# Optimization experiments

Measured on AMD Instinct MI355X. Metric: run time of the kernel, lower is better.

Reference implementation:

```python
import jax, jax.numpy as jnp
import numpy as np
import math

MIN_NORM = 1e-15
EPS = 1e-7
MAX_NORM = 1e6

N = 100000      # num nodes (aaa)
E = 1600000     # num edges
D_IN = 129      # embedding_num (1 time coord + 128 spatial)
D_OUT = 128     # output1_dim
MAXLEN = 50
B = 4096
NCLASS = 5

# ---------------- Hyperboloid manifold ops (HGCN-style) ----------------

def proj(x, c):
    K = 1. / c
    y = x[..., 1:]
    y_sq = jnp.sum(y * y, axis=-1, keepdims=True)
    x0 = jnp.sqrt(jnp.clip(K + y_sq, EPS))
    return jnp.concatenate([x0, y], axis=-1)

def proj_tan0(u, c):
    # zero out the time coordinate
    return jnp.concatenate([jnp.zeros_like(u[..., :1]), u[..., 1:]], axis=-1)

def expmap0(u, c):
    K = 1. / c
    sqrtK = jnp.sqrt(K)
    x = u[..., 1:]
    xn = jnp.maximum(jnp.linalg.norm(x, axis=-1, keepdims=True), MIN_NORM)
    theta = xn / sqrtK
    first = sqrtK * jnp.cosh(theta)
    rest = sqrtK * jnp.sinh(theta) * x / xn
    return proj(jnp.concatenate([first, rest], axis=-1), c)

def logmap0(x, c):
    K = 1. / c
    sqrtK = jnp.sqrt(K)
    y = x[..., 1:]
    yn = jnp.maximum(jnp.linalg.norm(y, axis=-1, keepdims=True), MIN_NORM)
    theta = jnp.clip(x[..., 0:1] / sqrtK, 1.0 + EPS)
    rest = sqrtK * jnp.arccosh(theta) * y / yn
    return jnp.concatenate([jnp.zeros_like(theta), rest], axis=-1)

def minkowski_dot(x, y):
    return jnp.sum(x * y, axis=-1, keepdims=True) - 2.0 * x[..., 0:1] * y[..., 0:1]

def minkowski_norm(u):
    return jnp.sqrt(jnp.clip(minkowski_dot(u, u), EPS))

def expmap(u, x, c):
    K = 1. / c
    sqrtK = jnp.sqrt(K)
    normu = jnp.minimum(minkowski_norm(u), MAX_NORM)
    theta = jnp.maximum(normu / sqrtK, MIN_NORM)
    result = jnp.cosh(theta) * x + jnp.sinh(theta) * u / theta
    return proj(result, c)

def proj_tan(u, x, c):
    ux = jnp.sum(x[..., 1:] * u[..., 1:], axis=-1, keepdims=True)
    vals0 = ux / jnp.clip(x[..., 0:1], EPS)
    return jnp.concatenate([vals0, u[..., 1:]], axis=-1)

def ptransp0(x, u, c):
    K = 1. / c
    sqrtK = jnp.sqrt(K)
    x0 = x[..., 0:1]
    y = x[..., 1:]
    yn = jnp.maximum(jnp.linalg.norm(y, axis=-1, keepdims=True), MIN_NORM)
    yhat = y / yn
    v = jnp.concatenate([-yn, (sqrtK - x0) * yhat], axis=-1)
    alpha = jnp.sum(yhat * u[..., 1:], axis=-1, keepdims=True) / sqrtK
    return proj_tan(u - alpha * v, x, c)

def mobius_add(x, y, c):
    u = logmap0(y, c)
    v = ptransp0(x, jnp.broadcast_to(u, x.shape), c)
    return expmap(v, x, c)

def mobius_add0(x, y, c):
    # tangent-space addition at the origin
    return expmap0(logmap0(x, c) + logmap0(y, c), c)

def mobius_matvec1(m, x, c):
    return expmap0(logmap0(x, c) @ m, c)

def mobius_matvec0(n, x, c):
    # per-row scalar mobius scaling (n is (N,1))
    return expmap0(n * logmap0(x, c), c)

def hyp_bias_point(b, c):
    return proj(expmap0(proj_tan0(b[None, :], c), c), c)

def gcn_layer(x, w, b, rows, cols, vals, c, n_nodes):
    out = mobius_matvec1(w, x, c)
    out = mobius_add(out, hyp_bias_point(b, c), c)
    out = logmap0(out, c)
    out = jax.ops.segment_sum(vals[:, None] * out[cols], rows, num_segments=n_nodes)
    return proj(expmap0(out, c), c)


def setup_inputs() -> dict:
    key = jax.random.key(0)
    ks = jax.random.split(key, 20)
    def ku(k, shape, fan_in):
        bound = 1.0 / math.sqrt(fan_in)
        return jax.random.uniform(k, shape, jnp.float32, -bound, bound)
    inp = {}
    inp['A1_tensor'] = jax.random.normal(ks[0], (N, D_IN), jnp.float32)
    inp['adj_rows'] = jax.random.randint(ks[1], (E,), 0, N)
    inp['adj_cols'] = jax.random.randint(ks[2], (E,), 0, N)
    inp['adj_vals'] = jax.random.uniform(ks[3], (E,), jnp.float32) * 0.1
    inp['batch_idx'] = jax.random.randint(ks[4], (B, 1, MAXLEN), 0, N)
    inp['raw_c'] = jnp.array([math.log(math.exp(1.0) - 1.0)], jnp.float32)
    inp['n_param'] = jax.random.uniform(ks[5], (N, 1), jnp.float32)
    inp['Lin1'] = ku(ks[6], (D_IN, D_OUT), D_IN)
    inp['Lin1_bias'] = ku(ks[7], (D_OUT,), D_IN)
    inp['gc1_w'] = ku(ks[8], (D_IN, D_OUT), D_IN)
    inp['gc1_b'] = ku(ks[9], (D_OUT,), D_IN)
    inp['gc2_w'] = ku(ks[10], (D_OUT, D_OUT), D_OUT)
    inp['gc2_b'] = ku(ks[11], (D_OUT,), D_OUT)
    inp['weight'] = ku(ks[12], (D_OUT, MAXLEN), D_OUT)
    inp['weight2'] = ku(ks[13], (D_OUT, MAXLEN), D_OUT)
    inp['conv1_w'] = ku(ks[14], (MAXLEN,), MAXLEN)
    inp['conv1_b'] = ku(ks[15], (1,), MAXLEN)
    inp['conv2_w'] = ku(ks[16], (MAXLEN,), MAXLEN)
    inp['conv2_b'] = ku(ks[17], (1,), MAXLEN)
    inp['classifier'] = ku(ks[18], (2 * MAXLEN, NCLASS), 2 * MAXLEN)
    inp['classifier_bias'] = ku(ks[19], (NCLASS,), 2 * MAXLEN)
    return inp


def reference(A1_tensor, adj_rows, adj_cols, adj_vals, batch_idx, raw_c, n_param,
              Lin1, Lin1_bias, gc1_w, gc1_b, gc2_w, gc2_b, weight, weight2,
              conv1_w, conv1_b, conv2_w, conv2_b, classifier, classifier_bias):
    c = jax.nn.softplus(raw_c)[0] + 1e-5
    bi = batch_idx[:, 0, :]                       # (B, L)
    flat = bi.reshape(-1)

    x_tan = proj_tan0(A1_tensor, c)
    a = proj(expmap0(x_tan, c), c)                # (N, D_IN)

    a1 = mobius_matvec1(Lin1, a, c)               # (N, D_OUT)
    a1 = mobius_add(a1, hyp_bias_point(Lin1_bias, c), c)
    a2 = mobius_matvec0(n_param, a1, c)

    x_1 = gcn_layer(a, gc1_w, gc1_b, adj_rows, adj_cols, adj_vals, c, N)
    x_1 = mobius_matvec0(1.0 - n_param, x_1, c)
    x_1 = mobius_add0(x_1, a2, c)
    x_2 = gcn_layer(x_1, gc2_w, gc2_b, adj_rows, adj_cols, adj_vals, c, N)

    # readout branch 1: x_2 gathered on batch indices
    s2 = logmap0(x_2[flat].reshape(bi.shape[0], bi.shape[1], D_OUT), c)  # (B,L,D)
    s2 = jnp.einsum('bld,dt->blt', s2, weight)    # (B, L, MAXLEN)
    s2 = jnp.einsum('blt,l->bt', s2, conv1_w) + conv1_b  # kernel-size-1 conv over channels

    # readout branch 2: a1 gathered on batch indices
    s3 = logmap0(a1[flat].reshape(bi.shape[0], bi.shape[1], D_OUT), c)
    s3 = jnp.einsum('bld,dt->blt', s3, weight2)
    s3 = jnp.einsum('blt,l->bt', s3, conv2_w) + conv2_b

    sel = jnp.concatenate([s2, s3], axis=1)       # (B, 2*MAXLEN)
    pre = sel @ classifier + classifier_bias      # (B, NCLASS)
    return jnp.argmax(pre, axis=-1), sel
```

## Files before the change

### kernel.cpp

```cpp
#include <hip/hip_runtime.h>
#include <math.h>


typedef unsigned short ushort_t;
typedef __attribute__((ext_vector_type(8))) short short8;
typedef __attribute__((ext_vector_type(4))) float f32x4;
typedef __attribute__((ext_vector_type(4))) unsigned short u16x4;

__device__ __forceinline__ float wsum(float x){
  x += __shfl_xor(x, 32);
  x += __shfl_xor(x, 16);
  x += __shfl_xor(x, 8);
  x += __shfl_xor(x, 4);
  x += __shfl_xor(x, 2);
  x += __shfl_xor(x, 1);
  return x;
}

__device__ __forceinline__ void get_c(const float* rc, float& K, float& sK){
  float c = log1pf(expf(rc[0])) + 1e-5f;
  K  = 1.0f / c;
  sK = sqrtf(K);
}

__device__ __forceinline__ float sinhx_over_x(float x){
  if (x > 1e-3f){
    float e  = __expf(x);
    float em = __builtin_amdgcn_rcpf(e);
    return 0.5f*(e - em) * __builtin_amdgcn_rcpf(x);
  }
  return 1.0f + x*x*(1.0f/6.0f);
}

__device__ __forceinline__ float facosh(float x){
  return __logf(x + sqrtf(fmaxf(fmaf(x, x, -1.0f), 0.0f)));
}

__device__ __forceinline__ ushort_t bf16_rne(float x){
  unsigned int u = __float_as_uint(x);
  u += 0x7fffu + ((u >> 16) & 1u);
  return (ushort_t)(u >> 16);
}
__device__ __forceinline__ float bf2f(ushort_t h){
  return __uint_as_float(((unsigned int)h) << 16);
}
__device__ __forceinline__ unsigned int pack_bf16(float x, float y){
  unsigned int bx = __float_as_uint(x);
  unsigned int by = __float_as_uint(y);
  bx = (bx + 0x7fffu + ((bx >> 16) & 1u)) >> 16;
  by = (by + 0x7fffu + ((by >> 16) & 1u)) & 0xffff0000u;
  return bx | by;
}
__device__ __forceinline__ float bf_lo(unsigned int p){ return __uint_as_float(p << 16); }
__device__ __forceinline__ float bf_hi(unsigned int p){ return __uint_as_float(p & 0xffff0000u); }

__device__ __forceinline__ void chain_scalars(float tt, float tu, float uu,
                                              float K, float sK,
                                              float& At, float& Au){
  float xn  = fmaxf(sqrtf(tt), 1e-15f);
  float th  = xn / sK;
  float f   = sinhx_over_x(th);
  float pn2 = f*f*tt;
  float p0  = sqrtf(fmaxf(K + pn2, 1e-7f));
  float S_yu = f * tu;
  float yn  = fmaxf(sqrtf(pn2), 1e-15f);
  float inv_yn = __builtin_amdgcn_rcpf(yn);
  float alpha = S_yu * inv_yn / sK;
  float coef  = alpha * (sK - p0);
  float cy  = coef * inv_yn;
  float cyf = cy * f;
  float pdw  = S_yu - cy*pn2;
  float spsq = uu - 2.f*cy*S_yu + cy*cy*pn2;
  float w0 = pdw / fmaxf(p0, 1e-7f);
  float md = spsq - w0*w0;
  float normu = fminf(sqrtf(fmaxf(md, 1e-7f)), 1e6f);
  float th2 = fmaxf(normu / sK, 1e-15f);
  float e  = __expf(th2);
  float em = __builtin_amdgcn_rcpf(e);
  float ch = 0.5f*(e + em);
  float g  = (th2 > 1e-3f) ? 0.5f*(e - em)*__builtin_amdgcn_rcpf(th2)
                           : 1.0f + th2*th2*(1.0f/6.0f);
  float rn2 = ch*ch*pn2 + 2.f*ch*g*pdw + g*g*spsq;
  float r0 = sqrtf(fmaxf(K + rn2, 1e-7f));
  float ynf = fmaxf(sqrtf(rn2), 1e-15f);
  float thf = fmaxf(r0/sK, 1.f+1e-7f);
  float rf = sK * facosh(thf) * __builtin_amdgcn_rcpf(ynf);
  At = rf*(ch*f - g*cyf);
  Au = rf*g;
}

__global__ __launch_bounds__(256) void prep(const int* __restrict__ rows,
                                            int* __restrict__ cnt,
                                            int* __restrict__ rnk, int e,
                                            const float* __restrict__ A1,
                                            ushort_t* __restrict__ Lhi,
                                            ushort_t* __restrict__ Llo,
                                            const float* __restrict__ Lin1,
                                            const float* __restrict__ G1,
                                            const float* __restrict__ G2,
                                            ushort_t* __restrict__ Wb,
                                            const float* __restrict__ b0,
                                            const float* __restrict__ b1,
                                            const float* __restrict__ b2,
                                            float* __restrict__ uu3,
                                            int n, int histB, int sBlocks){
  int bid = blockIdx.x;
  if (bid < histB){
    int base = (bid * 256 + threadIdx.x) * 4;
    if (base + 3 < e){
      int4 r = *(const int4*)&rows[base];
      int k0 = atomicAdd(&cnt[r.x], 1);
      int k1 = atomicAdd(&cnt[r.y], 1);
      int k2 = atomicAdd(&cnt[r.z], 1);
      int k3 = atomicAdd(&cnt[r.w], 1);
      *(int4*)&rnk[base] = make_int4(k0, k1, k2, k3);
    } else {
      for (int i = base; i < e; ++i) rnk[i] = atomicAdd(&cnt[rows[i]], 1);
    }
  } else if (bid < histB + sBlocks){
    int sb = bid - histB;
    size_t i4 = (size_t)sb * 256 + threadIdx.x;
    size_t tot4 = (size_t)n * 32;
    if (i4 < tot4){
      size_t row = i4 >> 5; int j0 = (int)(i4 & 31) * 4;
      const float* s = A1 + row*129 + 1 + j0;
      float v0 = s[0], v1 = s[1], v2 = s[2], v3 = s[3];
      ushort_t h0 = bf16_rne(v0), h1 = bf16_rne(v1), h2 = bf16_rne(v2), h3 = bf16_rne(v3);
      u16x4 hh = {h0, h1, h2, h3};
      u16x4 ll = {bf16_rne(v0 - bf2f(h0)), bf16_rne(v1 - bf2f(h1)),
                  bf16_rne(v2 - bf2f(h2)), bf16_rne(v3 - bf2f(h3))};
      *(u16x4*)&Lhi[i4*4] = hh;
      *(u16x4*)&Llo[i4*4] = ll;
    }
    if (sb == 0 && threadIdx.x < 64){
      int lane = threadIdx.x;
      const float* bs[3] = {b0, b1, b2};
      for (int k = 0; k < 3; ++k){
        float x = lane ? bs[k][2*lane] : 0.0f;
        float y = bs[k][2*lane+1];
        float s = wsum(x*x + y*y);
        if (lane == 0) uu3[k] = s;
      }
    }
  } else {
    int wb = bid - histB - sBlocks;
    int which = wb >> 6, b = wb & 63;
    const float* W = (which == 0) ? (Lin1 + 128) : (which == 1) ? (G1 + 128) : G2;
    ushort_t* Whi = Wb + (size_t)which * 2 * 16384;
    ushort_t* Wlo = Whi + 16384;
    int id = b * 256 + threadIdx.x;
    int k = id >> 7, nn = id & 127;
    float v = W[(size_t)k*128 + nn];
    ushort_t h = bf16_rne(v);
    Whi[(size_t)nn*128 + k] = h;
    Wlo[(size_t)nn*128 + k] = bf16_rne(v - bf2f(h));
  }
}

__global__ __launch_bounds__(256) void mfma_chain(const ushort_t* __restrict__ Ahi,
                                                  const ushort_t* __restrict__ Alo,
                                                  const ushort_t* __restrict__ Whi,
                                                  const ushort_t* __restrict__ Wlo,
                                                  const float* __restrict__ bias,
                                                  const float* __restrict__ uu3, int uuidx,
                                                  const float* __restrict__ raw_c,
                                                  float* __restrict__ outF,
                                                  unsigned int* __restrict__ outH,
                                                  int mode, int n, int nWaves){
  __shared__ ushort_t Wsh[2][128*128];
  int tid = threadIdx.x;
  {
    const uint4* gh = (const uint4*)Whi;
    const uint4* gl = (const uint4*)Wlo;
    uint4* sh = (uint4*)Wsh[0];
    uint4* sl = (uint4*)Wsh[1];
    #pragma unroll
    for (int i = 0; i < 8; ++i){
      int idx = tid + 256*i;
      int sw = idx ^ ((idx >> 4) & 7);
      sh[sw] = gh[idx];
    }
    #pragma unroll
    for (int i = 0; i < 8; ++i){
      int idx = tid + 256*i;
      int sw = idx ^ ((idx >> 4) & 7);
      sl[sw] = gl[idx];
    }
  }
  __syncthreads();

  int lane = tid & 63;
  int c = lane & 15, quad = lane >> 4;
  int wid = blockIdx.x * 4 + (tid >> 6);
  int nStrips = (n + 15) >> 4;
  int csw = (c & 7) << 3;

  float K, sK; get_c(raw_c, K, sK);
  float uu = uu3[uuidx];
  float uv[8];
  #pragma unroll
  for (int t = 0; t < 8; ++t){
    int col = t*16 + c;
    uv[t] = (col == 0) ? 0.f : bias[col];
  }

  for (int strip = wid; strip < nStrips; strip += nWaves){
    int m0 = strip * 16;
    int ra = m0 + c; if (ra > n - 1) ra = n - 1;
    short8 ahi[4], alo[4];
    #pragma unroll
    for (int kc = 0; kc < 4; ++kc){
      size_t aoff = (size_t)ra*128 + kc*32 + quad*8;
      ahi[kc] = *(const short8*)&Ahi[aoff];
      alo[kc] = *(const short8*)&Alo[aoff];
    }

    f32x4 acc[8];
    #pragma unroll
    for (int t = 0; t < 8; ++t){
      f32x4 z = {0.f, 0.f, 0.f, 0.f};
      acc[t] = z;
      int wrow = (t*16 + c) * 128;
      #pragma unroll
      for (int kc = 0; kc < 4; ++kc){
        int woff = (wrow + kc*32 + quad*8) ^ csw;
        short8 bhi = *(const short8*)&Wsh[0][woff];
        short8 blo = *(const short8*)&Wsh[1][woff];
        acc[t] = __builtin_amdgcn_mfma_f32_16x16x32_bf16(ahi[kc], bhi, acc[t], 0, 0, 0);
        acc[t] = __builtin_amdgcn_mfma_f32_16x16x32_bf16(ahi[kc], blo, acc[t], 0, 0, 0);
        acc[t] = __builtin_amdgcn_mfma_f32_16x16x32_bf16(alo[kc], bhi, acc[t], 0, 0, 0);
      }
    }

    if (c == 0){
      f32x4 z = {0.f, 0.f, 0.f, 0.f};
      acc[0] = z;
    }
    #pragma unroll
    for (int r = 0; r < 4; ++r){
      float tt = 0.f, tu = 0.f;
      #pragma unroll
      for (int t = 0; t < 8; ++t){
        float v = acc[t][r];
        tt = fmaf(v, v, tt);
        tu = fmaf(v, uv[t], tu);
      }
      #pragma unroll
      for (int m = 1; m <= 8; m <<= 1){
        tt += __shfl_xor(tt, m);
        tu += __shfl_xor(tu, m);
      }
      float At, Au; chain_scalars(tt, tu, uu, K, sK, At, Au);
      int row = m0 + quad*4 + r;
      if (mode == 0){
        if (row < n){
          #pragma unroll
          for (int t = 0; t < 8; ++t){
            float o = fmaf(At, acc[t][r], Au*uv[t]);
            outF[(size_t)row*128 + t*16 + c] = o;
          }
        }
      } else {
        #pragma unroll
        for (int t = 0; t < 8; ++t){
          float o  = fmaf(At, acc[t][r], Au*uv[t]);
          float on = __shfl_xor(o, 1);
          if (row < n && !(c & 1))
            outH[(size_t)row*64 + t*8 + (c >> 1)] = pack_bf16(o, on);
        }
      }
    }
  }
}

#define SCAN_ITEMS 4
__global__ __launch_bounds__(256) void scan1(const int* __restrict__ cnt,
                                             int* __restrict__ off,
                                             int* __restrict__ bsum, int n){
  __shared__ int sh[256];
  int tid = threadIdx.x;
  int base = blockIdx.x * 256 * SCAN_ITEMS + tid * SCAN_ITEMS;
  int v[SCAN_ITEMS]; int s = 0;
  #pragma unroll
  for (int i = 0; i < SCAN_ITEMS; ++i){ int idx = base+i; v[i] = (idx < n) ? cnt[idx] : 0; s += v[i]; }
  sh[tid] = s; __syncthreads();
  for (int o = 1; o < 256; o <<= 1){
    int t = (tid >= o) ? sh[tid - o] : 0; __syncthreads();
    sh[tid] += t; __syncthreads();
  }
  int excl = sh[tid] - s;
  if (tid == 255) bsum[blockIdx.x] = sh[tid];
  int run = excl;
  #pragma unroll
  for (int i = 0; i < SCAN_ITEMS; ++i){ int idx = base+i; if (idx < n) off[idx] = run; run += v[i]; }
}

__global__ __launch_bounds__(256) void scan2(int* __restrict__ bsum, int G){
  __shared__ int sh[256];
  int t = threadIdx.x;
  int v = (t < G) ? bsum[t] : 0;
  sh[t] = v; __syncthreads();
  for (int o = 1; o < 256; o <<= 1){
    int x = (t >= o) ? sh[t - o] : 0; __syncthreads();
    sh[t] += x; __syncthreads();
  }
  if (t < G) bsum[t] = sh[t] - v;
}

__global__ __launch_bounds__(256) void fill_k(const int* __restrict__ rows,
                                              const int* __restrict__ cols,
                                              const float* __restrict__ vals,
                                              const int* __restrict__ off,
                                              const int* __restrict__ bsum,
                                              const int* __restrict__ rnk,
                                              int2* __restrict__ ecv, int e){
  int base = (blockIdx.x * 256 + threadIdx.x) * 4;
  if (base + 3 < e){
    int4   r = *(const int4*)&rows[base];
    int4   q = *(const int4*)&rnk[base];
    int4   c = *(const int4*)&cols[base];
    float4 v = *(const float4*)&vals[base];
    int o0 = off[r.x] + bsum[r.x >> 10];
    int o1 = off[r.y] + bsum[r.y >> 10];
    int o2 = off[r.z] + bsum[r.z >> 10];
    int o3 = off[r.w] + bsum[r.w >> 10];
    ecv[o0 + q.x] = make_int2(c.x, __float_as_int(v.x));
    ecv[o1 + q.y] = make_int2(c.y, __float_as_int(v.y));
    ecv[o2 + q.z] = make_int2(c.z, __float_as_int(v.z));
    ecv[o3 + q.w] = make_int2(c.w, __float_as_int(v.w));
  } else {
    for (int i = base; i < e; ++i)
      ecv[off[rows[i]] + bsum[rows[i] >> 10] + rnk[i]] = make_int2(cols[i], __float_as_int(vals[i]));
  }
}

__device__ __forceinline__ float2 seg_gather_bf16(const unsigned int* __restrict__ h,
                                                  const int* __restrict__ off,
                                                  const int* __restrict__ bsum,
                                                  const int* __restrict__ cnt,
                                                  const int2* __restrict__ ecv,
                                                  int row, int lane){
  float ax = 0.f, ay = 0.f, bx = 0.f, by = 0.f;
  int st = off[row] + bsum[row >> 10], deg = cnt[row];
  const unsigned int* __restrict__ hb = h + lane;
  for (int b = 0; b < deg; b += 64){
    int k = b + lane;
    int cc = 0; float vv = 0.f;
    if (k < deg){ int2 e = ecv[st+k]; cc = e.x; vv = __int_as_float(e.y); }
    int m = min(64, deg - b);
    for (int j = 0; j < m; j += 8){
      int   c0=__shfl(cc,j+0), c1=__shfl(cc,j+1), c2=__shfl(cc,j+2), c3=__shfl(cc,j+3);
      int   c4=__shfl(cc,j+4), c5=__shfl(cc,j+5), c6=__shfl(cc,j+6), c7=__shfl(cc,j+7);
      float v0=__shfl(vv,j+0), v1=__shfl(vv,j+1), v2=__shfl(vv,j+2), v3=__shfl(vv,j+3);
      float v4=__shfl(vv,j+4), v5=__shfl(vv,j+5), v6=__shfl(vv,j+6), v7=__shfl(vv,j+7);
      unsigned int p0 = hb[(size_t)c0*64];
      unsigned int p1 = hb[(size_t)c1*64];
      unsigned int p2 = hb[(size_t)c2*64];
      unsigned int p3 = hb[(size_t)c3*64];
      unsigned int p4 = hb[(size_t)c4*64];
      unsigned int p5 = hb[(size_t)c5*64];
      unsigned int p6 = hb[(size_t)c6*64];
      unsigned int p7 = hb[(size_t)c7*64];
      ax = fmaf(v0, bf_lo(p0), ax); ay = fmaf(v0, bf_hi(p0), ay);
      bx = fmaf(v1, bf_lo(p1), bx); by = fmaf(v1, bf_hi(p1), by);
      ax = fmaf(v2, bf_lo(p2), ax); ay = fmaf(v2, bf_hi(p2), ay);
      bx = fmaf(v3, bf_lo(p3), bx); by = fmaf(v3, bf_hi(p3), by);
      ax = fmaf(v4, bf_lo(p4), ax); ay = fmaf(v4, bf_hi(p4), ay);
      bx = fmaf(v5, bf_lo(p5), bx); by = fmaf(v5, bf_hi(p5), by);
      ax = fmaf(v6, bf_lo(p6), ax); ay = fmaf(v6, bf_hi(p6), ay);
      bx = fmaf(v7, bf_lo(p7), bx); by = fmaf(v7, bf_hi(p7), by);
    }
  }
  return make_float2(ax + bx, ay + by);
}

__global__ __launch_bounds__(256) void seg_x1(const unsigned int* __restrict__ h1,
                                              const int* __restrict__ off,
                                              const int* __restrict__ bsum,
                                              const int* __restrict__ cnt,
                                              const int2* __restrict__ ecv,
                                              const float* __restrict__ loga1,
                                              const float* __restrict__ nparam,
                                              unsigned int* __restrict__ X1hi,
                                              unsigned int* __restrict__ X1lo, int n){
  int row  = (int)((blockIdx.x * blockDim.x + threadIdx.x) >> 6);
  int lane = threadIdx.x & 63;
  if (row >= n) return;
  float2 acc = seg_gather_bf16(h1, off, bsum, cnt, ecv, row, lane);
  float nv = nparam[row];
  float2 la1 = *(const float2*)&loga1[(size_t)row*128 + 2*lane];
  float ox = (1.f-nv)*acc.x + nv*la1.x;
  float oy = (1.f-nv)*acc.y + nv*la1.y;
  unsigned int hp = pack_bf16(ox, oy);
  X1hi[(size_t)row*64 + lane] = hp;
  X1lo[(size_t)row*64 + lane] = pack_bf16(ox - bf_lo(hp), oy - bf_hi(hp));
}

__global__ __launch_bounds__(256) void seg_x2(const unsigned int* __restrict__ h2,
                                              const int* __restrict__ off,
                                              const int* __restrict__ bsum,
                                              const int* __restrict__ cnt,
                                              const int2* __restrict__ ecv,
                                              unsigned int* __restrict__ Lx2p, int n){
  int row  = (int)((blockIdx.x * blockDim.x + threadIdx.x) >> 6);
  int lane = threadIdx.x & 63;
  if (row >= n) return;
  float2 acc = seg_gather_bf16(h2, off, bsum, cnt, ecv, row, lane);
  Lx2p[(size_t)row*64 + lane] = pack_bf16(acc.x, acc.y);
}

__global__ __launch_bounds__(128) void batch_head(const unsigned int* __restrict__ Lx2p,
                                                  const float* __restrict__ loga1,
                                                  const int* __restrict__ bidx,
                                                  const float* __restrict__ weight,
                                                  const float* __restrict__ weight2,
                                                  const float* __restrict__ c1w,
                                                  const float* __restrict__ c1b,
                                                  const float* __restrict__ c2w,
                                                  const float* __restrict__ c2b,
                                                  const float* __restrict__ cls,
                                                  const float* __restrict__ clsb,
                                                  float* __restrict__ out, int Bn){
  __shared__ float sg2[128], sg3[128], ssel[100], spre[5];
  __shared__ int sbi[50];
  __shared__ float sc1[50], sc2[50];
  int b = blockIdx.x, d = threadIdx.x;
  const int* bi = bidx + (size_t)b * 50;
  if (d < 50){ sbi[d] = bi[d]; sc1[d] = c1w[d]; sc2[d] = c2w[d]; }
  __syncthreads();
  int lane = d & 63;
  bool lo = d < 64;
  float gx = 0.f, gy = 0.f;
  if (lo){
    const unsigned int* __restrict__ tp = Lx2p + lane;
    #pragma unroll
    for (int l = 0; l < 50; l += 5){
      int i0 = sbi[l+0], i1 = sbi[l+1], i2 = sbi[l+2], i3 = sbi[l+3], i4 = sbi[l+4];
      unsigned int p0 = tp[(size_t)i0*64];
      unsigned int p1 = tp[(size_t)i1*64];
      unsigned int p2 = tp[(size_t)i2*64];
      unsigned int p3 = tp[(size_t)i3*64];
      unsigned int p4 = tp[(size_t)i4*64];
      float w0 = sc1[l+0], w1 = sc1[l+1], w2 = sc1[l+2], w3 = sc1[l+3], w4 = sc1[l+4];
      gx = fmaf(w0, bf_lo(p0), gx); gy = fmaf(w0, bf_hi(p0), gy);
      gx = fmaf(w1, bf_lo(p1), gx); gy = fmaf(w1, bf_hi(p1), gy);
      gx = fmaf(w2, bf_lo(p2), gx); gy = fmaf(w2, bf_hi(p2), gy);
      gx = fmaf(w3, bf_lo(p3), gx); gy = fmaf(w3, bf_hi(p3), gy);
      gx = fmaf(w4, bf_lo(p4), gx); gy = fmaf(w4, bf_hi(p4), gy);
    }
    sg2[2*lane] = gx; sg2[2*lane+1] = gy;
  } else {
    const float2* __restrict__ t2 = (const float2*)loga1 + lane;
    #pragma unroll
    for (int l = 0; l < 50; l += 5){
      int i0 = sbi[l+0], i1 = sbi[l+1], i2 = sbi[l+2], i3 = sbi[l+3], i4 = sbi[l+4];
      float2 p0 = t2[(size_t)i0*64];
      float2 p1 = t2[(size_t)i1*64];
      float2 p2 = t2[(size_t)i2*64];
      float2 p3 = t2[(size_t)i3*64];
      float2 p4 = t2[(size_t)i4*64];
      float w0 = sc2[l+0], w1 = sc2[l+1], w2 = sc2[l+2], w3 = sc2[l+3], w4 = sc2[l+4];
      gx = fmaf(w0, p0.x, gx); gy = fmaf(w0, p0.y, gy);
      gx = fmaf(w1, p1.x, gx); gy = fmaf(w1, p1.y, gy);
      gx = fmaf(w2, p2.x, gx); gy = fmaf(w2, p2.y, gy);
      gx = fmaf(w3, p3.x, gx); gy = fmaf(w3, p3.y, gy);
      gx = fmaf(w4, p4.x, gx); gy = fmaf(w4, p4.y, gy);
    }
    sg3[2*lane] = gx; sg3[2*lane+1] = gy;
  }
  __syncthreads();
  if (d < 50){
    float s = 0.f;
    for (int k = 0; k < 128; ++k) s = fmaf(sg2[k], weight[k*50 + d], s);
    s += c1b[0];
    ssel[d] = s;
    out[(size_t)Bn + (size_t)b*100 + d] = s;
  } else if (d >= 64 && d < 114){
    int t = d - 64;
    float s = 0.f;
    for (int k = 0; k < 128; ++k) s = fmaf(sg3[k], weight2[k*50 + t], s);
    s += c2b[0];
    ssel[50 + t] = s;
    out[(size_t)Bn + (size_t)b*100 + 50 + t] = s;
  }
  __syncthreads();
  if (d < 5){
    float s = clsb[d];
    for (int j = 0; j < 100; ++j) s = fmaf(ssel[j], cls[j*5 + d], s);
    spre[d] = s;
  }
  __syncthreads();
  if (d == 0){
    int best = 0; float bv = spre[0];
    #pragma unroll
    for (int k = 1; k < 5; ++k) if (spre[k] > bv){ bv = spre[k]; best = k; }
    out[b] = (float)best;
  }
}

extern "C" void kernel_launch(void* const* d_in, const int* in_sizes, int n_in,
                              void* d_out, int out_size, void* d_ws, size_t ws_size,
                              hipStream_t stream) {
  const float* A1     = (const float*)d_in[0];
  const int*   rows   = (const int*)  d_in[1];
  const int*   cols   = (const int*)  d_in[2];
  const float* vals   = (const float*)d_in[3];
  const int*   bidx   = (const int*)  d_in[4];
  const float* raw_c  = (const float*)d_in[5];
  const float* nparam = (const float*)d_in[6];
  const float* Lin1   = (const float*)d_in[7];
  const float* Lin1_b = (const float*)d_in[8];
  const float* gc1_w  = (const float*)d_in[9];
  const float* gc1_b  = (const float*)d_in[10];
  const float* gc2_w  = (const float*)d_in[11];
  const float* gc2_b  = (const float*)d_in[12];
  const float* weight = (const float*)d_in[13];
  const float* weight2= (const float*)d_in[14];
  const float* c1w    = (const float*)d_in[15];
  const float* c1b    = (const float*)d_in[16];
  const float* c2w    = (const float*)d_in[17];
  const float* c2b    = (const float*)d_in[18];
  const float* cls    = (const float*)d_in[19];
  const float* clsb   = (const float*)d_in[20];

  int N  = in_sizes[0] / 129;
  int E  = in_sizes[1];
  int Bn = in_sizes[4] / 50;
  size_t NF = (size_t)N * 128;

  ushort_t* Lhi = (ushort_t*)d_ws;
  ushort_t* Llo = Lhi + NF;
  unsigned int* Lx2p = (unsigned int*)d_ws;
  float*    S3  = (float*)(Llo + NF);
  unsigned int* Hb   = (unsigned int*)(S3 + NF);
  unsigned int* X1hi = Hb + NF/2;
  unsigned int* X1lo = X1hi + NF/2;
  ushort_t* Wb = (ushort_t*)(X1lo + NF/2);
  ushort_t* W1h = Wb,           *W1l = Wb + 16384;
  ushort_t* W2h = Wb + 2*16384, *W2l = Wb + 3*16384;
  ushort_t* W3h = Wb + 4*16384, *W3l = Wb + 5*16384;
  int* cnt    = (int*)(Wb + 6*16384);
  int* off    = cnt + N;
  int* rnk    = off + N;
  int* bsum   = rnk + E;
  int2* ecv   = (int2*)(bsum + 4096);
  float* uu3  = (float*)(ecv + E);

  int rowBlocks  = (N + 3) / 4;
  int G = (N + 256*SCAN_ITEMS - 1) / (256*SCAN_ITEMS);
  int histB = (E/4 + 255) / 256 + 1;
  int sBlocks = (int)(((size_t)N*32 + 255)/256);
  int mBlocks = 512;
  int nWaves  = mBlocks * 4;

  hipMemsetAsync(cnt, 0, (size_t)N*sizeof(int), stream);
  prep<<<histB + sBlocks + 192, 256, 0, stream>>>(rows, cnt, rnk, E,
                                                  A1, Lhi, Llo,
                                                  Lin1, gc1_w, gc2_w, Wb,
                                                  Lin1_b, gc1_b, gc2_b, uu3,
                                                  N, histB, sBlocks);
  scan1<<<G, 256, 0, stream>>>(cnt, off, bsum, N);
  scan2<<<1, 256, 0, stream>>>(bsum, G);
  fill_k<<<histB, 256, 0, stream>>>(rows, cols, vals, off, bsum, rnk, ecv, E);

  mfma_chain<<<mBlocks, 256, 0, stream>>>(Lhi, Llo, W1h, W1l, Lin1_b, uu3, 0, raw_c,
                                          S3, (unsigned int*)nullptr, 0, N, nWaves);
  mfma_chain<<<mBlocks, 256, 0, stream>>>(Lhi, Llo, W2h, W2l, gc1_b, uu3, 1, raw_c,
                                          (float*)nullptr, Hb, 1, N, nWaves);
  seg_x1<<<rowBlocks, 256, 0, stream>>>(Hb, off, bsum, cnt, ecv, S3, nparam,
                                        X1hi, X1lo, N);
  mfma_chain<<<mBlocks, 256, 0, stream>>>((const ushort_t*)X1hi, (const ushort_t*)X1lo,
                                          W3h, W3l, gc2_b, uu3, 2, raw_c,
                                          (float*)nullptr, Hb, 1, N, nWaves);
  seg_x2<<<rowBlocks, 256, 0, stream>>>(Hb, off, bsum, cnt, ecv, Lx2p, N);
  batch_head<<<Bn, 128, 0, stream>>>(Lx2p, S3, bidx, weight, weight2, c1w, c1b,
                                     c2w, c2b, cls, clsb, (float*)d_out, Bn);
}
```

Before: 563.1 us.

## Fuse CSR fill with first two MFMA GEMMs into one interleaved launch

```diff
diff --git a/kernel.cpp b/kernel.cpp
--- a/kernel.cpp
+++ b/kernel.cpp
@@ -157,46 +157,19 @@
   }
 }
 
-__global__ __launch_bounds__(256) void mfma_chain(const ushort_t* __restrict__ Ahi,
-                                                  const ushort_t* __restrict__ Alo,
-                                                  const ushort_t* __restrict__ Whi,
-                                                  const ushort_t* __restrict__ Wlo,
-                                                  const float* __restrict__ bias,
-                                                  const float* __restrict__ uu3, int uuidx,
-                                                  const float* __restrict__ raw_c,
-                                                  float* __restrict__ outF,
-                                                  unsigned int* __restrict__ outH,
-                                                  int mode, int n, int nWaves){
-  __shared__ ushort_t Wsh[2][128*128];
-  int tid = threadIdx.x;
-  {
-    const uint4* gh = (const uint4*)Whi;
-    const uint4* gl = (const uint4*)Wlo;
-    uint4* sh = (uint4*)Wsh[0];
-    uint4* sl = (uint4*)Wsh[1];
-    #pragma unroll
-    for (int i = 0; i < 8; ++i){
-      int idx = tid + 256*i;
-      int sw = idx ^ ((idx >> 4) & 7);
-      sh[sw] = gh[idx];
-    }
-    #pragma unroll
-    for (int i = 0; i < 8; ++i){
-      int idx = tid + 256*i;
-      int sw = idx ^ ((idx >> 4) & 7);
-      sl[sw] = gl[idx];
-    }
-  }
-  __syncthreads();
-
-  int lane = tid & 63;
+__device__ __forceinline__ void gemm_strips(const ushort_t* __restrict__ Ahi,
+                                            const ushort_t* __restrict__ Alo,
+                                            const ushort_t* __restrict__ Wsh0,
+                                            const ushort_t* __restrict__ Wsh1,
+                                            const float* __restrict__ bias,
+                                            float uu, float K, float sK,
+                                            float* __restrict__ outF,
+                                            unsigned int* __restrict__ outH,
+                                            int mode, int n, int wid, int nWaves,
+                                            int lane){
   int c = lane & 15, quad = lane >> 4;
-  int wid = blockIdx.x * 4 + (tid >> 6);
   int nStrips = (n + 15) >> 4;
   int csw = (c & 7) << 3;
-
-  float K, sK; get_c(raw_c, K, sK);
-  float uu = uu3[uuidx];
   float uv[8];
   #pragma unroll
   for (int t = 0; t < 8; ++t){
@@ -224,8 +197,8 @@
       #pragma unroll
       for (int kc = 0; kc < 4; ++kc){
         int woff = (wrow + kc*32 + quad*8) ^ csw;
-        short8 bhi = *(const short8*)&Wsh[0][woff];
-        short8 blo = *(const short8*)&Wsh[1][woff];
+        short8 bhi = *(const short8*)&Wsh0[woff];
+        short8 blo = *(const short8*)&Wsh1[woff];
         acc[t] = __builtin_amdgcn_mfma_f32_16x16x32_bf16(ahi[kc], bhi, acc[t], 0, 0, 0);
         acc[t] = __builtin_amdgcn_mfma_f32_16x16x32_bf16(ahi[kc], blo, acc[t], 0, 0, 0);
         acc[t] = __builtin_amdgcn_mfma_f32_16x16x32_bf16(alo[kc], bhi, acc[t], 0, 0, 0);
@@ -273,6 +246,125 @@
   }
 }
 
+__global__ __launch_bounds__(256) void fillm12(const int* __restrict__ rows,
+                                               const int* __restrict__ cols,
+                                               const float* __restrict__ vals,
+                                               const int* __restrict__ off,
+                                               const int* __restrict__ bsum,
+                                               const int* __restrict__ rnk,
+                                               int2* __restrict__ ecv, int e,
+                                               const ushort_t* __restrict__ Ahi,
+                                               const ushort_t* __restrict__ Alo,
+                                               const ushort_t* __restrict__ Wb,
+                                               const float* __restrict__ bias1,
+                                               const float* __restrict__ bias2,
+                                               const float* __restrict__ uu3,
+                                               const float* __restrict__ raw_c,
+                                               float* __restrict__ outF,
+                                               unsigned int* __restrict__ outH,
+                                               int n, int M, int T){
+  __shared__ ushort_t Wsh[2][128*128];
+  int bid = blockIdx.x;
+  long mlo = ((long)bid * M) / T;
+  long mhi = ((long)(bid + 1) * M) / T;
+
+  if (mhi == mlo){
+    int fblk = bid - (int)mlo;
+    int base = (fblk * 256 + threadIdx.x) * 4;
+    if (base + 3 < e){
+      int4   r = *(const int4*)&rows[base];
+      int4   q = *(const int4*)&rnk[base];
+      int4   c = *(const int4*)&cols[base];
+      float4 v = *(const float4*)&vals[base];
+      int o0 = off[r.x] + bsum[r.x >> 10];
+      int o1 = off[r.y] + bsum[r.y >> 10];
+      int o2 = off[r.z] + bsum[r.z >> 10];
+      int o3 = off[r.w] + bsum[r.w >> 10];
+      ecv[o0 + q.x] = make_int2(c.x, __float_as_int(v.x));
+      ecv[o1 + q.y] = make_int2(c.y, __float_as_int(v.y));
+      ecv[o2 + q.z] = make_int2(c.z, __float_as_int(v.z));
+      ecv[o3 + q.w] = make_int2(c.w, __float_as_int(v.w));
+    } else {
+      for (int i = base; i < e; ++i)
+        ecv[off[rows[i]] + bsum[rows[i] >> 10] + rnk[i]] = make_int2(cols[i], __float_as_int(vals[i]));
+    }
+    return;
+  }
+
+  int mblk = (int)mlo;
+  int role = mblk >> 9;
+  int rblk = mblk & 511;
+  const ushort_t* Whi = Wb + (size_t)role * 2 * 16384;
+  const ushort_t* Wlo = Whi + 16384;
+  int tid = threadIdx.x;
+  {
+    const uint4* gh = (const uint4*)Whi;
+    const uint4* gl = (const uint4*)Wlo;
+    uint4* sh = (uint4*)Wsh[0];
+    uint4* sl = (uint4*)Wsh[1];
+    #pragma unroll
+    for (int i = 0; i < 8; ++i){
+      int idx = tid + 256*i;
+      int sw = idx ^ ((idx >> 4) & 7);
+      sh[sw] = gh[idx];
+    }
+    #pragma unroll
+    for (int i = 0; i < 8; ++i){
+      int idx = tid + 256*i;
+      int sw = idx ^ ((idx >> 4) & 7);
+      sl[sw] = gl[idx];
+    }
+  }
+  __syncthreads();
+
+  float K, sK; get_c(raw_c, K, sK);
+  float uu = uu3[role];
+  int wid = rblk * 4 + (tid >> 6);
+  gemm_strips(Ahi, Alo, Wsh[0], Wsh[1],
+              role == 0 ? bias1 : bias2, uu, K, sK,
+              role == 0 ? outF : nullptr,
+              role == 0 ? nullptr : outH,
+              role, n, wid, 2048, tid & 63);
+}
+
+__global__ __launch_bounds__(256) void mfma_chain(const ushort_t* __restrict__ Ahi,
+                                                  const ushort_t* __restrict__ Alo,
+                                                  const ushort_t* __restrict__ Whi,
+                                                  const ushort_t* __restrict__ Wlo,
+                                                  const float* __restrict__ bias,
+                                                  const float* __restrict__ uu3, int uuidx,
+                                                  const float* __restrict__ raw_c,
+                                                  unsigned int* __restrict__ outH,
+                                                  int n, int nWaves){
+  __shared__ ushort_t Wsh[2][128*128];
+  int tid = threadIdx.x;
+  {
+    const uint4* gh = (const uint4*)Whi;
+    const uint4* gl = (const uint4*)Wlo;
+    uint4* sh = (uint4*)Wsh[0];
+    uint4* sl = (uint4*)Wsh[1];
+    #pragma unroll
+    for (int i = 0; i < 8; ++i){
+      int idx = tid + 256*i;
+      int sw = idx ^ ((idx >> 4) & 7);
+      sh[sw] = gh[idx];
+    }
+    #pragma unroll
+    for (int i = 0; i < 8; ++i){
+      int idx = tid + 256*i;
+      int sw = idx ^ ((idx >> 4) & 7);
+      sl[sw] = gl[idx];
+    }
+  }
+  __syncthreads();
+
+  float K, sK; get_c(raw_c, K, sK);
+  float uu = uu3[uuidx];
+  int wid = blockIdx.x * 4 + (tid >> 6);
+  gemm_strips(Ahi, Alo, Wsh[0], Wsh[1], bias, uu, K, sK,
+              nullptr, outH, 1, n, wid, nWaves, tid & 63);
+}
+
 #define SCAN_ITEMS 4
 __global__ __launch_bounds__(256) void scan1(const int* __restrict__ cnt,
                                              int* __restrict__ off,
@@ -307,40 +399,13 @@
   if (t < G) bsum[t] = sh[t] - v;
 }
 
-__global__ __launch_bounds__(256) void fill_k(const int* __restrict__ rows,
-                                              const int* __restrict__ cols,
-                                              const float* __restrict__ vals,
-                                              const int* __restrict__ off,
-                                              const int* __restrict__ bsum,
-                                              const int* __restrict__ rnk,
-                                              int2* __restrict__ ecv, int e){
-  int base = (blockIdx.x * 256 + threadIdx.x) * 4;
-  if (base + 3 < e){
-    int4   r = *(const int4*)&rows[base];
-    int4   q = *(const int4*)&rnk[base];
-    int4   c = *(const int4*)&cols[base];
-    float4 v = *(const float4*)&vals[base];
-    int o0 = off[r.x] + bsum[r.x >> 10];
-    int o1 = off[r.y] + bsum[r.y >> 10];
-    int o2 = off[r.z] + bsum[r.z >> 10];
-    int o3 = off[r.w] + bsum[r.w >> 10];
-    ecv[o0 + q.x] = make_int2(c.x, __float_as_int(v.x));
-    ecv[o1 + q.y] = make_int2(c.y, __float_as_int(v.y));
-    ecv[o2 + q.z] = make_int2(c.z, __float_as_int(v.z));
-    ecv[o3 + q.w] = make_int2(c.w, __float_as_int(v.w));
-  } else {
-    for (int i = base; i < e; ++i)
-      ecv[off[rows[i]] + bsum[rows[i] >> 10] + rnk[i]] = make_int2(cols[i], __float_as_int(vals[i]));
-  }
-}
-
 __device__ __forceinline__ float2 seg_gather_bf16(const unsigned int* __restrict__ h,
                                                   const int* __restrict__ off,
                                                   const int* __restrict__ bsum,
                                                   const int* __restrict__ cnt,
                                                   const int2* __restrict__ ecv,
                                                   int row, int lane){
-  float ax = 0.f, ay = 0.f, bx = 0.f, by = 0.f;
+  float a0x=0.f,a0y=0.f,a1x=0.f,a1y=0.f,a2x=0.f,a2y=0.f,a3x=0.f,a3y=0.f;
   int st = off[row] + bsum[row >> 10], deg = cnt[row];
   const unsigned int* __restrict__ hb = h + lane;
   for (int b = 0; b < deg; b += 64){
@@ -348,30 +413,50 @@
     int cc = 0; float vv = 0.f;
     if (k < deg){ int2 e = ecv[st+k]; cc = e.x; vv = __int_as_float(e.y); }
     int m = min(64, deg - b);
-    for (int j = 0; j < m; j += 8){
-      int   c0=__shfl(cc,j+0), c1=__shfl(cc,j+1), c2=__shfl(cc,j+2), c3=__shfl(cc,j+3);
-      int   c4=__shfl(cc,j+4), c5=__shfl(cc,j+5), c6=__shfl(cc,j+6), c7=__shfl(cc,j+7);
-      float v0=__shfl(vv,j+0), v1=__shfl(vv,j+1), v2=__shfl(vv,j+2), v3=__shfl(vv,j+3);
-      float v4=__shfl(vv,j+4), v5=__shfl(vv,j+5), v6=__shfl(vv,j+6), v7=__shfl(vv,j+7);
-      unsigned int p0 = hb[(size_t)c0*64];
-      unsigned int p1 = hb[(size_t)c1*64];
-      unsigned int p2 = hb[(size_t)c2*64];
-      unsigned int p3 = hb[(size_t)c3*64];
-      unsigned int p4 = hb[(size_t)c4*64];
-      unsigned int p5 = hb[(size_t)c5*64];
-      unsigned int p6 = hb[(size_t)c6*64];
-      unsigned int p7 = hb[(size_t)c7*64];
-      ax = fmaf(v0, bf_lo(p0), ax); ay = fmaf(v0, bf_hi(p0), ay);
-      bx = fmaf(v1, bf_lo(p1), bx); by = fmaf(v1, bf_hi(p1), by);
-      ax = fmaf(v2, bf_lo(p2), ax); ay = fmaf(v2, bf_hi(p2), ay);
-      bx = fmaf(v3, bf_lo(p3), bx); by = fmaf(v3, bf_hi(p3), by);
-      ax = fmaf(v4, bf_lo(p4), ax); ay = fmaf(v4, bf_hi(p4), ay);
-      bx = fmaf(v5, bf_lo(p5), bx); by = fmaf(v5, bf_hi(p5), by);
-      ax = fmaf(v6, bf_lo(p6), ax); ay = fmaf(v6, bf_hi(p6), ay);
-      bx = fmaf(v7, bf_lo(p7), bx); by = fmaf(v7, bf_hi(p7), by);
-    }
-  }
-  return make_float2(ax + bx, ay + by);
+    for (int j = 0; j < m; j += 16){
+      int   c0 =__shfl(cc,j+0),  c1 =__shfl(cc,j+1),  c2 =__shfl(cc,j+2),  c3 =__shfl(cc,j+3);
+      int   c4 =__shfl(cc,j+4),  c5 =__shfl(cc,j+5),  c6 =__shfl(cc,j+6),  c7 =__shfl(cc,j+7);
+      int   c8 =__shfl(cc,j+8),  c9 =__shfl(cc,j+9),  c10=__shfl(cc,j+10), c11=__shfl(cc,j+11);
+      int   c12=__shfl(cc,j+12), c13=__shfl(cc,j+13), c14=__shfl(cc,j+14), c15=__shfl(cc,j+15);
+      float v0 =__shfl(vv,j+0),  v1 =__shfl(vv,j+1),  v2 =__shfl(vv,j+2),  v3 =__shfl(vv,j+3);
+      float v4 =__shfl(vv,j+4),  v5 =__shfl(vv,j+5),  v6 =__shfl(vv,j+6),  v7 =__shfl(vv,j+7);
+      float v8 =__shfl(vv,j+8),  v9 =__shfl(vv,j+9),  v10=__shfl(vv,j+10), v11=__shfl(vv,j+11);
+      float v12=__shfl(vv,j+12), v13=__shfl(vv,j+13), v14=__shfl(vv,j+14), v15=__shfl(vv,j+15);
+      unsigned int p0  = hb[(size_t)c0 *64];
+      unsigned int p1  = hb[(size_t)c1 *64];
+      unsigned int p2  = hb[(size_t)c2 *64];
+      unsigned int p3  = hb[(size_t)c3 *64];
+      unsigned int p4  = hb[(size_t)c4 *64];
+      unsigned int p5  = hb[(size_t)c5 *64];
+      unsigned int p6  = hb[(size_t)c6 *64];
+      unsigned int p7  = hb[(size_t)c7 *64];
+      unsigned int p8  = hb[(size_t)c8 *64];
+      unsigned int p9  = hb[(size_t)c9 *64];
+      unsigned int p10 = hb[(size_t)c10*64];
+      unsigned int p11 = hb[(size_t)c11*64];
+      unsigned int p12 = hb[(size_t)c12*64];
+      unsigned int p13 = hb[(size_t)c13*64];
+      unsigned int p14 = hb[(size_t)c14*64];
+      unsigned int p15 = hb[(size_t)c15*64];
+      a0x = fmaf(v0,  bf_lo(p0),  a0x); a0y = fmaf(v0,  bf_hi(p0),  a0y);
+      a1x = fmaf(v1,  bf_lo(p1),  a1x); a1y = fmaf(v1,  bf_hi(p1),  a1y);
+      a2x = fmaf(v2,  bf_lo(p2),  a2x); a2y = fmaf(v2,  bf_hi(p2),  a2y);
+      a3x = fmaf(v3,  bf_lo(p3),  a3x); a3y = fmaf(v3,  bf_hi(p3),  a3y);
+      a0x = fmaf(v4,  bf_lo(p4),  a0x); a0y = fmaf(v4,  bf_hi(p4),  a0y);
+      a1x = fmaf(v5,  bf_lo(p5),  a1x); a1y = fmaf(v5,  bf_hi(p5),  a1y);
+      a2x = fmaf(v6,  bf_lo(p6),  a2x); a2y = fmaf(v6,  bf_hi(p6),  a2y);
+      a3x = fmaf(v7,  bf_lo(p7),  a3x); a3y = fmaf(v7,  bf_hi(p7),  a3y);
+      a0x = fmaf(v8,  bf_lo(p8),  a0x); a0y = fmaf(v8,  bf_hi(p8),  a0y);
+      a1x = fmaf(v9,  bf_lo(p9),  a1x); a1y = fmaf(v9,  bf_hi(p9),  a1y);
+      a2x = fmaf(v10, bf_lo(p10), a2x); a2y = fmaf(v10, bf_hi(p10), a2y);
+      a3x = fmaf(v11, bf_lo(p11), a3x); a3y = fmaf(v11, bf_hi(p11), a3y);
+      a0x = fmaf(v12, bf_lo(p12), a0x); a0y = fmaf(v12, bf_hi(p12), a0y);
+      a1x = fmaf(v13, bf_lo(p13), a1x); a1y = fmaf(v13, bf_hi(p13), a1y);
+      a2x = fmaf(v14, bf_lo(p14), a2x); a2y = fmaf(v14, bf_hi(p14), a2y);
+      a3x = fmaf(v15, bf_lo(p15), a3x); a3y = fmaf(v15, bf_hi(p15), a3y);
+    }
+  }
+  return make_float2((a0x + a1x) + (a2x + a3x), (a0y + a1y) + (a2y + a3y));
 }
 
 __global__ __launch_bounds__(256) void seg_x1(const unsigned int* __restrict__ h1,
@@ -536,8 +621,6 @@
   unsigned int* X1hi = Hb + NF/2;
   unsigned int* X1lo = X1hi + NF/2;
   ushort_t* Wb = (ushort_t*)(X1lo + NF/2);
-  ushort_t* W1h = Wb,           *W1l = Wb + 16384;
-  ushort_t* W2h = Wb + 2*16384, *W2l = Wb + 3*16384;
   ushort_t* W3h = Wb + 4*16384, *W3l = Wb + 5*16384;
   int* cnt    = (int*)(Wb + 6*16384);
   int* off    = cnt + N;
@@ -550,8 +633,8 @@
   int G = (N + 256*SCAN_ITEMS - 1) / (256*SCAN_ITEMS);
   int histB = (E/4 + 255) / 256 + 1;
   int sBlocks = (int)(((size_t)N*32 + 255)/256);
-  int mBlocks = 512;
-  int nWaves  = mBlocks * 4;
+  int M = 1024;
+  int T = histB + M;
 
   hipMemsetAsync(cnt, 0, (size_t)N*sizeof(int), stream);
   prep<<<histB + sBlocks + 192, 256, 0, stream>>>(rows, cnt, rnk, E,
@@ -561,17 +644,15 @@
                                                   N, histB, sBlocks);
   scan1<<<G, 256, 0, stream>>>(cnt, off, bsum, N);
   scan2<<<1, 256, 0, stream>>>(bsum, G);
-  fill_k<<<histB, 256, 0, stream>>>(rows, cols, vals, off, bsum, rnk, ecv, E);
-
-  mfma_chain<<<mBlocks, 256, 0, stream>>>(Lhi, Llo, W1h, W1l, Lin1_b, uu3, 0, raw_c,
-                                          S3, (unsigned int*)nullptr, 0, N, nWaves);
-  mfma_chain<<<mBlocks, 256, 0, stream>>>(Lhi, Llo, W2h, W2l, gc1_b, uu3, 1, raw_c,
-                                          (float*)nullptr, Hb, 1, N, nWaves);
+
+  fillm12<<<T, 256, 0, stream>>>(rows, cols, vals, off, bsum, rnk, ecv, E,
+                                 Lhi, Llo, Wb, Lin1_b, gc1_b, uu3, raw_c,
+                                 S3, Hb, N, M, T);
   seg_x1<<<rowBlocks, 256, 0, stream>>>(Hb, off, bsum, cnt, ecv, S3, nparam,
                                         X1hi, X1lo, N);
-  mfma_chain<<<mBlocks, 256, 0, stream>>>((const ushort_t*)X1hi, (const ushort_t*)X1lo,
-                                          W3h, W3l, gc2_b, uu3, 2, raw_c,
-                                          (float*)nullptr, Hb, 1, N, nWaves);
+  mfma_chain<<<512, 256, 0, stream>>>((const ushort_t*)X1hi, (const ushort_t*)X1lo,
+                                      W3h, W3l, gc2_b, uu3, 2, raw_c,
+                                      Hb, N, 512*4);
   seg_x2<<<rowBlocks, 256, 0, stream>>>(Hb, off, bsum, cnt, ecv, Lx2p, N);
   batch_head<<<Bn, 128, 0, stream>>>(Lx2p, S3, bidx, weight, weight2, c1w, c1b,
                                      c2w, c2b, cls, clsb, (float*)d_out, Bn);
```

After: 567.4 us. Within noise of the previous version (+0.8%).
